# Kernel optimization log

Measured on AMD Instinct MI355X. Metric: run time of the kernel, lower is better.

Reference implementation:

```python
import jax, jax.numpy as jnp
import numpy as np

S, T, D, H = 16384, 16, 128, 3   # statements, AST nodes per statement, feat dim, heads
N = S * T
EPS = 1e-5


def setup_inputs() -> dict:
    key = jax.random.key(0)
    k = jax.random.split(key, 12)
    idx = np.arange(N)
    child = idx[idx % T != 0]                      # chain edges child->parent within each AST
    src = jnp.asarray(np.concatenate([child, idx]), dtype=jnp.int32)       # + self loops
    dst = jnp.asarray(np.concatenate([child - 1, idx]), dtype=jnp.int32)
    sD = 1.0 / np.sqrt(D)
    s3D = 1.0 / np.sqrt(3.0 * D)
    return dict(
        x=jax.random.normal(k[0], (N, D), jnp.float32),
        W0=jax.random.normal(k[1], (D, H * D), jnp.float32) * sD,
        a_src0=jax.random.normal(k[2], (H, D), jnp.float32) * sD,
        a_dst0=jax.random.normal(k[3], (H, D), jnp.float32) * sD,
        b0=jnp.zeros((H * D,), jnp.float32),
        g0=jnp.ones((H * D,), jnp.float32),
        be0=jnp.zeros((H * D,), jnp.float32),
        W1=jax.random.normal(k[4], (H * D, D), jnp.float32) * s3D,
        a_src1=jax.random.normal(k[5], (1, D), jnp.float32) * sD,
        a_dst1=jax.random.normal(k[6], (1, D), jnp.float32) * sD,
        b1=jnp.zeros((D,), jnp.float32),
        g1=jnp.ones((D,), jnp.float32),
        be1=jnp.zeros((D,), jnp.float32),
        p=jax.random.normal(k[7], (D,), jnp.float32),
        mW1=jax.random.normal(k[8], (D, 32), jnp.float32) * sD,
        mb1=jnp.zeros((32,), jnp.float32),
        mW2=jax.random.normal(k[9], (32, D), jnp.float32) / np.sqrt(32.0),
        mb2=jnp.zeros((D,), jnp.float32),
        src=src,
        dst=dst,
    )


def _gat(x, W, a_s, a_d, b, src, dst, heads, out_c):
    # PyG GATConv (concat heads, leaky_relu 0.2, self-loops already in edge list)
    h = (x @ W).reshape(-1, heads, out_c)                 # [N,H,C]
    al_s = jnp.einsum('nhc,hc->nh', h, a_s)
    al_d = jnp.einsum('nhc,hc->nh', h, a_d)
    e = jax.nn.leaky_relu(al_s[src] + al_d[dst], 0.2)     # [E,H]
    m = jax.ops.segment_max(e, dst, num_segments=N)       # segment softmax over incoming edges
    ex = jnp.exp(e - m[dst])
    den = jax.ops.segment_sum(ex, dst, num_segments=N)
    alpha = ex / den[dst]
    out = jax.ops.segment_sum(alpha[:, :, None] * h[src], dst, num_segments=N)
    return out.reshape(-1, heads * out_c) + b


def _bn(x, g, b):
    mu = x.mean(0)
    var = x.var(0)
    return (x - mu) * jax.lax.rsqrt(var + EPS) * g + b


def reference(x, W0, a_src0, a_dst0, b0, g0, be0, W1, a_src1, a_dst1, b1, g1, be1, p, mW1, mb1, mW2, mb2, src, dst):
    h = _bn(jax.nn.relu(_gat(x, W0, a_src0, a_dst0, b0, src, dst, H, D)), g0, be0)
    h = _bn(jax.nn.relu(_gat(h, W1, a_src1, a_dst1, b1, src, dst, 1, D)), g1, be1)
    # TopKPooling (default ratio=0.5) per statement AST of T nodes
    s = (h @ p) / (jnp.linalg.norm(p) + 1e-16)            # [N]
    s = s.reshape(S, T)
    k = T // 2
    vals, idxk = jax.lax.top_k(s, k)                      # [S,k]
    hr = h.reshape(S, T, D)
    sel = jnp.take_along_axis(hr, idxk[:, :, None], axis=1) * jnp.tanh(vals)[:, :, None]
    pooled = jax.nn.relu(sel).mean(axis=1)                # [S,D] readout of kept nodes
    out = jax.nn.relu(pooled @ mW1 + mb1) @ mW2 + mb2     # MLP 128->32->128
    return out
```

## Files before the change

kernel.cpp:

```cpp
#include <hip/hip_runtime.h>
#include <math.h>

#define N_NODES 262144
#define SSTMT   16384
#define TT      16
#define DD      128
#define HH      3
#define HD      384
#define EPSV    1e-5f

__device__ __forceinline__ void stage64x128(float (*dst)[128], const float* __restrict__ src)
{
    const int tid = threadIdx.x;
    #pragma unroll
    for (int j = 0; j < 8; ++j) {
        int gi = j * 256 + tid;
        int row = gi >> 5;
        int col = (gi & 31) * 4;
        *reinterpret_cast<float4*>(&dst[row][col]) =
            *reinterpret_cast<const float4*>(&src[(size_t)row * DD + col]);
    }
}

#define FMA16(av, b0, b1, b2, b3, ai)                                   \
    acc[ai][0] += av.x * b0.x; acc[ai][1] += av.x * b0.y;               \
    acc[ai][2] += av.x * b0.z; acc[ai][3] += av.x * b0.w;               \
    acc[ai][0] += av.y * b1.x; acc[ai][1] += av.y * b1.y;               \
    acc[ai][2] += av.y * b1.z; acc[ai][3] += av.y * b1.w;               \
    acc[ai][0] += av.z * b2.x; acc[ai][1] += av.z * b2.y;               \
    acc[ai][2] += av.z * b2.z; acc[ai][3] += av.z * b2.w;               \
    acc[ai][0] += av.w * b3.x; acc[ai][1] += av.w * b3.y;               \
    acc[ai][2] += av.w * b3.z; acc[ai][3] += av.w * b3.w;

template<int BSTR>
__device__ __forceinline__ void gemm128_lA(const float (*A)[128],
                                           const float* __restrict__ Bg,
                                           int rg, int c4, float acc[8][4])
{
    const float* bp = Bg + c4;
    #pragma unroll 4
    for (int k = 0; k < 128; k += 4) {
        float4 b0 = *reinterpret_cast<const float4*>(bp);
        float4 b1 = *reinterpret_cast<const float4*>(bp + BSTR);
        float4 b2 = *reinterpret_cast<const float4*>(bp + 2 * BSTR);
        float4 b3 = *reinterpret_cast<const float4*>(bp + 3 * BSTR);
        bp += 4 * BSTR;
        #pragma unroll
        for (int i = 0; i < 8; ++i) {
            float4 av = *reinterpret_cast<const float4*>(&A[rg * 8 + i][k]);
            FMA16(av, b0, b1, b2, b3, i)
        }
    }
}

__device__ __forceinline__ void attn_reg(const float acc[8][4],
                                         float4 av_s, float4 av_d,
                                         int rg, float aS[8], float aN[8])
{
    float als_t[8], ald_t[8];
    #pragma unroll
    for (int i = 0; i < 8; ++i) {
        als_t[i] = acc[i][0] * av_s.x + acc[i][1] * av_s.y
                 + acc[i][2] * av_s.z + acc[i][3] * av_s.w;
        ald_t[i] = acc[i][0] * av_d.x + acc[i][1] * av_d.y
                 + acc[i][2] * av_d.z + acc[i][3] * av_d.w;
    }
    #pragma unroll
    for (int m = 1; m <= 16; m <<= 1) {
        #pragma unroll
        for (int i = 0; i < 8; ++i) {
            als_t[i] += __shfl_xor(als_t[i], m);
            ald_t[i] += __shfl_xor(ald_t[i], m);
        }
    }
    float alsN = __shfl_down(als_t[0], 32);
    const bool rgodd = (rg & 1);
    #pragma unroll
    for (int i = 0; i < 8; ++i) {
        float es = als_t[i] + ald_t[i];
        es = es > 0.f ? es : 0.2f * es;
        float aSv = 1.f, aNv = 0.f;
        if (!(rgodd && i == 7)) {
            float en = ((i < 7) ? als_t[i + 1] : alsN) + ald_t[i];
            en = en > 0.f ? en : 0.2f * en;
            float mx = fmaxf(es, en);
            float xse = expf(es - mx), xne = expf(en - mx);
            float den = xse + xne;
            aSv = xse / den; aNv = xne / den;
        }
        aS[i] = aSv; aN[i] = aNv;
    }
}

__global__ __launch_bounds__(256, 4)
void gat0_stats(const float* __restrict__ x, const float* __restrict__ W0,
                const float* __restrict__ as0, const float* __restrict__ ad0,
                const float* __restrict__ b0, float* __restrict__ pA0)
{
    __shared__ float xs[64][128];

    const int tid = threadIdx.x;
    const int bid = blockIdx.x;
    const int rg = tid >> 5;
    const int c4 = (tid & 31) * 4;
    const size_t rb = (size_t)bid * 64;

    stage64x128(xs, x + rb * DD);
    __syncthreads();

    float psum[HH][4], qsum[HH][4];
    #pragma unroll
    for (int h = 0; h < HH; ++h)
        #pragma unroll
        for (int j = 0; j < 4; ++j) { psum[h][j] = 0.f; qsum[h][j] = 0.f; }

    for (int h = 0; h < HH; ++h) {
        float acc[8][4];
        #pragma unroll
        for (int i = 0; i < 8; ++i)
            #pragma unroll
            for (int j = 0; j < 4; ++j) acc[i][j] = 0.f;

        gemm128_lA<HD>(xs, W0 + h * DD, rg, c4, acc);

        float4 avS = *reinterpret_cast<const float4*>(&as0[h * DD + c4]);
        float4 avD = *reinterpret_cast<const float4*>(&ad0[h * DD + c4]);
        float aS[8], aN[8];
        attn_reg(acc, avS, avD, rg, aS, aN);

        float accN[4];
        #pragma unroll
        for (int j = 0; j < 4; ++j) accN[j] = __shfl_down(acc[0][j], 32);

        float4 bb = *reinterpret_cast<const float4*>(&b0[h * DD + c4]);
        float bbv[4] = {bb.x, bb.y, bb.z, bb.w};
        const bool rgodd = (rg & 1);
        #pragma unroll
        for (int i = 0; i < 8; ++i) {
            #pragma unroll
            for (int j = 0; j < 4; ++j) {
                float nbj = (i < 7) ? acc[i + 1][j] : (rgodd ? 0.f : accN[j]);
                float o = fmaxf(aS[i] * acc[i][j] + aN[i] * nbj + bbv[j], 0.f);
                psum[h][j] += o; qsum[h][j] += o * o;
            }
        }
    }

    float* bna = &xs[0][0];
    for (int h = 0; h < HH; ++h) {
        __syncthreads();
        #pragma unroll
        for (int j = 0; j < 4; ++j) {
            float s = psum[h][j] + __shfl_down(psum[h][j], 32);
            float q = qsum[h][j] + __shfl_down(qsum[h][j], 32);
            if ((tid & 63) < 32) {
                int w = tid >> 6;
                bna[w * 128 + c4 + j] = s;
                bna[512 + w * 128 + c4 + j] = q;
            }
        }
        __syncthreads();
        if (tid < 128) {
            float s = bna[tid] + bna[128 + tid] + bna[256 + tid] + bna[384 + tid];
            float q = bna[512 + tid] + bna[640 + tid] + bna[768 + tid] + bna[896 + tid];
            size_t idx = ((size_t)bid * HD + h * DD + tid) * 2;
            pA0[idx] = s; pA0[idx + 1] = q;
        }
    }
}

__global__ __launch_bounds__(256, 2)
void gat1_recomp(const float* __restrict__ x, const float* __restrict__ W0,
                 const float* __restrict__ as0, const float* __restrict__ ad0,
                 const float* __restrict__ b0, const float* __restrict__ sc0,
                 const float* __restrict__ sh0, const float* __restrict__ W1,
                 const float* __restrict__ as1, const float* __restrict__ ad1,
                 const float* __restrict__ b1,
                 float* __restrict__ r1, float* __restrict__ pA1)
{
    __shared__ float xs[64][128];
    __shared__ float hs[64][128];

    const int tid = threadIdx.x;
    const int bid = blockIdx.x;
    const int rg = tid >> 5;
    const int c4 = (tid & 31) * 4;
    const size_t rb = (size_t)bid * 64;
    const bool rgodd = (rg & 1);

    stage64x128(xs, x + rb * DD);
    __syncthreads();

    float acc2[8][4];
    #pragma unroll
    for (int i = 0; i < 8; ++i)
        #pragma unroll
        for (int j = 0; j < 4; ++j) acc2[i][j] = 0.f;

    for (int h = 0; h < HH; ++h) {
        float acc[8][4];
        #pragma unroll
        for (int i = 0; i < 8; ++i)
            #pragma unroll
            for (int j = 0; j < 4; ++j) acc[i][j] = 0.f;

        gemm128_lA<HD>(xs, W0 + h * DD, rg, c4, acc);

        float4 avS = *reinterpret_cast<const float4*>(&as0[h * DD + c4]);
        float4 avD = *reinterpret_cast<const float4*>(&ad0[h * DD + c4]);
        float aS[8], aN[8];
        attn_reg(acc, avS, avD, rg, aS, aN);

        float accN[4];
        #pragma unroll
        for (int j = 0; j < 4; ++j) accN[j] = __shfl_down(acc[0][j], 32);

        float4 bb  = *reinterpret_cast<const float4*>(&b0[h * DD + c4]);
        float4 scv = *reinterpret_cast<const float4*>(&sc0[h * DD + c4]);
        float4 shv = *reinterpret_cast<const float4*>(&sh0[h * DD + c4]);
        float bbv[4]  = {bb.x, bb.y, bb.z, bb.w};
        float scvv[4] = {scv.x, scv.y, scv.z, scv.w};
        float shvv[4] = {shv.x, shv.y, shv.z, shv.w};
        float rr[8][4];
        #pragma unroll
        for (int i = 0; i < 8; ++i) {
            #pragma unroll
            for (int j = 0; j < 4; ++j) {
                float nbj = (i < 7) ? acc[i + 1][j] : (rgodd ? 0.f : accN[j]);
                float o = fmaxf(aS[i] * acc[i][j] + aN[i] * nbj + bbv[j], 0.f);
                rr[i][j] = o * scvv[j] + shvv[j];
            }
        }

        __syncthreads();
        #pragma unroll
        for (int i = 0; i < 8; ++i) {
            float4 v; v.x = rr[i][0]; v.y = rr[i][1]; v.z = rr[i][2]; v.w = rr[i][3];
            *reinterpret_cast<float4*>(&hs[rg * 8 + i][c4]) = v;
        }
        __syncthreads();

        gemm128_lA<DD>(hs, W1 + (size_t)h * DD * DD, rg, c4, acc2);
    }

    float4 avS1 = *reinterpret_cast<const float4*>(&as1[c4]);
    float4 avD1 = *reinterpret_cast<const float4*>(&ad1[c4]);
    float aS[8], aN[8];
    attn_reg(acc2, avS1, avD1, rg, aS, aN);

    float accN[4];
    #pragma unroll
    for (int j = 0; j < 4; ++j) accN[j] = __shfl_down(acc2[0][j], 32);

    float4 bb1 = *reinterpret_cast<const float4*>(&b1[c4]);
    float bb1v[4] = {bb1.x, bb1.y, bb1.z, bb1.w};
    float ps1[4] = {0, 0, 0, 0}, pq1[4] = {0, 0, 0, 0};
    #pragma unroll
    for (int i = 0; i < 8; ++i) {
        float ov[4];
        #pragma unroll
        for (int j = 0; j < 4; ++j) {
            float nbj = (i < 7) ? acc2[i + 1][j] : (rgodd ? 0.f : accN[j]);
            float o = fmaxf(aS[i] * acc2[i][j] + aN[i] * nbj + bb1v[j], 0.f);
            ov[j] = o;
            ps1[j] += o; pq1[j] += o * o;
        }
        float4 v; v.x = ov[0]; v.y = ov[1]; v.z = ov[2]; v.w = ov[3];
        *reinterpret_cast<float4*>(&r1[(rb + rg * 8 + i) * DD + c4]) = v;
    }

    float* bna = &xs[0][0];
    __syncthreads();
    #pragma unroll
    for (int j = 0; j < 4; ++j) {
        float s = ps1[j] + __shfl_down(ps1[j], 32);
        float q = pq1[j] + __shfl_down(pq1[j], 32);
        if ((tid & 63) < 32) {
            int w = tid >> 6;
            bna[w * 128 + c4 + j] = s;
            bna[512 + w * 128 + c4 + j] = q;
        }
    }
    __syncthreads();
    if (tid < 128) {
        float s = bna[tid] + bna[128 + tid] + bna[256 + tid] + bna[384 + tid];
        float q = bna[512 + tid] + bna[640 + tid] + bna[768 + tid] + bna[896 + tid];
        size_t idx = ((size_t)bid * DD + tid) * 2;
        pA1[idx] = s; pA1[idx + 1] = q;
    }
}

__global__ __launch_bounds__(256)
void bn_reduce(const float* __restrict__ pA, int nblk, int ncol, float invN,
               const float* __restrict__ g, const float* __restrict__ be,
               float* __restrict__ sc, float* __restrict__ sh)
{
    __shared__ float rs[256], rq[256];
    int col = blockIdx.x, tid = threadIdx.x;
    float s = 0.f, q = 0.f;
    for (int i = tid; i < nblk; i += 256) {
        size_t idx = ((size_t)i * ncol + col) * 2;
        s += pA[idx]; q += pA[idx + 1];
    }
    rs[tid] = s; rq[tid] = q;
    __syncthreads();
    for (int o = 128; o > 0; o >>= 1) {
        if (tid < o) { rs[tid] += rs[tid + o]; rq[tid] += rq[tid + o]; }
        __syncthreads();
    }
    if (tid == 0) {
        float mu  = rs[0] * invN;
        float var = fmaxf(rq[0] * invN - mu * mu, 0.f);
        float inv = 1.0f / sqrtf(var + EPSV);
        float scv = g[col] * inv;
        sc[col] = scv;
        sh[col] = be[col] - mu * scv;
    }
}

__global__ __launch_bounds__(128)
void compute_pn(const float* __restrict__ p, float* __restrict__ pn)
{
    __shared__ float rs[128];
    int t = threadIdx.x;
    float v = p[t];
    rs[t] = v * v;
    __syncthreads();
    for (int o = 64; o > 0; o >>= 1) {
        if (t < o) rs[t] += rs[t + o];
        __syncthreads();
    }
    float nrm = sqrtf(rs[0]) + 1e-16f;
    pn[t] = v / nrm;
}

__global__ __launch_bounds__(128)
void pool_mlp(const float* __restrict__ r1, const float* __restrict__ sc1,
              const float* __restrict__ sh1, const float* __restrict__ pn,
              const float* __restrict__ mW1, const float* __restrict__ mb1,
              const float* __restrict__ mW2, const float* __restrict__ mb2,
              float* __restrict__ out)
{
    __shared__ float hf[16][136];
    __shared__ float sv[16];
    __shared__ float tv[16];
    __shared__ float pooled[128];
    __shared__ float y1[32];
    int tid = threadIdx.x;
    int sid = blockIdx.x;
    float scv = sc1[tid], shv = sh1[tid];
    const float* base = r1 + (size_t)sid * TT * DD;
    #pragma unroll
    for (int i = 0; i < 16; ++i)
        hf[i][tid] = base[i * DD + tid] * scv + shv;
    __syncthreads();

    {
        int r = tid >> 3, q = tid & 7;
        float s = 0.f;
        #pragma unroll
        for (int cc = 0; cc < 16; ++cc) {
            int c = q + cc * 8;
            s += hf[r][c] * pn[c];
        }
        s += __shfl_down(s, 4, 8);
        s += __shfl_down(s, 2, 8);
        s += __shfl_down(s, 1, 8);
        if (q == 0) sv[r] = s;
    }
    __syncthreads();

    if (tid < 16) {
        float si = sv[tid];
        int rank = 0;
        #pragma unroll
        for (int u = 0; u < 16; ++u) {
            float su = sv[u];
            rank += (su > si || (su == si && u < tid)) ? 1 : 0;
        }
        tv[tid] = (rank < 8) ? tanhf(si) : 0.f;
    }
    __syncthreads();

    {
        float a = 0.f;
        #pragma unroll
        for (int rr = 0; rr < 16; ++rr)
            a += fmaxf(hf[rr][tid] * tv[rr], 0.f);
        pooled[tid] = a * 0.125f;
    }
    __syncthreads();

    {
        int j = tid >> 2, q = tid & 3;
        float a = 0.f;
        #pragma unroll
        for (int cc = 0; cc < 32; ++cc) {
            int c = q + cc * 4;
            a += pooled[c] * mW1[(size_t)c * 32 + j];
        }
        a += __shfl_down(a, 2, 4);
        a += __shfl_down(a, 1, 4);
        if (q == 0) y1[j] = fmaxf(a + mb1[j], 0.f);
    }
    __syncthreads();

    {
        float o = mb2[tid];
        #pragma unroll
        for (int j = 0; j < 32; ++j) o += y1[j] * mW2[j * 128 + tid];
        out[(size_t)sid * 128 + tid] = o;
    }
}

extern "C" void kernel_launch(void* const* d_in, const int* in_sizes, int n_in,
                              void* d_out, int out_size, void* d_ws, size_t ws_size,
                              hipStream_t stream)
{
    (void)in_sizes; (void)n_in; (void)out_size; (void)ws_size;
    const float* x   = (const float*)d_in[0];
    const float* W0  = (const float*)d_in[1];
    const float* as0 = (const float*)d_in[2];
    const float* ad0 = (const float*)d_in[3];
    const float* b0  = (const float*)d_in[4];
    const float* g0  = (const float*)d_in[5];
    const float* be0 = (const float*)d_in[6];
    const float* W1  = (const float*)d_in[7];
    const float* as1 = (const float*)d_in[8];
    const float* ad1 = (const float*)d_in[9];
    const float* b1  = (const float*)d_in[10];
    const float* g1  = (const float*)d_in[11];
    const float* be1 = (const float*)d_in[12];
    const float* p   = (const float*)d_in[13];
    const float* mW1 = (const float*)d_in[14];
    const float* mb1 = (const float*)d_in[15];
    const float* mW2 = (const float*)d_in[16];
    const float* mb2 = (const float*)d_in[17];
    float* out = (float*)d_out;

    const size_t R1B  = (size_t)N_NODES * DD * 4;
    const size_t PA0B = 4096ull * HD * 2 * 4;
    const size_t PA1B = 4096ull * DD * 2 * 4;

    char* ws = (char*)d_ws;
    float* r1  = (float*)ws;
    float* pA0 = (float*)(ws + R1B);
    float* pA1 = (float*)(ws + R1B + PA0B);
    float* vec = (float*)(ws + R1B + PA0B + PA1B);
    float* sc0 = vec;
    float* sh0 = vec + 512;
    float* sc1 = vec + 1024;
    float* sh1 = vec + 1536;
    float* pn  = vec + 2048;

    const float invN = 1.0f / (float)N_NODES;

    gat0_stats<<<N_NODES / 64, 256, 0, stream>>>(x, W0, as0, ad0, b0, pA0);
    bn_reduce<<<HD, 256, 0, stream>>>(pA0, N_NODES / 64, HD, invN, g0, be0, sc0, sh0);
    compute_pn<<<1, 128, 0, stream>>>(p, pn);
    gat1_recomp<<<N_NODES / 64, 256, 0, stream>>>(x, W0, as0, ad0, b0, sc0, sh0,
                                                  W1, as1, ad1, b1, r1, pA1);
    bn_reduce<<<DD, 256, 0, stream>>>(pA1, N_NODES / 64, DD, invN, g1, be1, sc1, sh1);
    pool_mlp<<<SSTMT, 128, 0, stream>>>(r1, sc1, sh1, pn, mW1, mb1, mW2, mb2, out);
}
```

Baseline: 1.296 ms.

## Use 8x8 register tiles with swizzled LDS and split-K in GAT kernels

Reworks the two fused GAT kernels so each thread computes an 8x8 output tile instead of 8x4, giving more FMAs per shared-memory and global load. The staged x and h tiles now use an XOR swizzle to avoid LDS bank conflicts. gat0_stats runs with 128 threads, and gat1_recomp splits K across two thread halves whose partial sums are combined through shared memory. This raises register pressure, adds extra barriers and split-K reduction traffic, and leaves only half the threads doing the attention epilogue in the second kernel.

```diff
diff --git a/kernel.cpp b/kernel.cpp
--- a/kernel.cpp
+++ b/kernel.cpp
@@ -9,163 +9,174 @@
 #define HD      384
 #define EPSV    1e-5f
 
-__device__ __forceinline__ void stage64x128(float (*dst)[128], const float* __restrict__ src)
+__device__ __forceinline__ int swzc(int row, int c) { return c ^ (((row >> 3) & 3) << 2); }
+
+template<int NTHR>
+__device__ __forceinline__ void stageSwz(float (*dst)[DD], const float* __restrict__ src)
 {
     const int tid = threadIdx.x;
     #pragma unroll
-    for (int j = 0; j < 8; ++j) {
-        int gi = j * 256 + tid;
+    for (int j = 0; j < 2048 / NTHR; ++j) {
+        int gi = j * NTHR + tid;
         int row = gi >> 5;
-        int col = (gi & 31) * 4;
-        *reinterpret_cast<float4*>(&dst[row][col]) =
-            *reinterpret_cast<const float4*>(&src[(size_t)row * DD + col]);
-    }
-}
-
-#define FMA16(av, b0, b1, b2, b3, ai)                                   \
-    acc[ai][0] += av.x * b0.x; acc[ai][1] += av.x * b0.y;               \
-    acc[ai][2] += av.x * b0.z; acc[ai][3] += av.x * b0.w;               \
-    acc[ai][0] += av.y * b1.x; acc[ai][1] += av.y * b1.y;               \
-    acc[ai][2] += av.y * b1.z; acc[ai][3] += av.y * b1.w;               \
-    acc[ai][0] += av.z * b2.x; acc[ai][1] += av.z * b2.y;               \
-    acc[ai][2] += av.z * b2.z; acc[ai][3] += av.z * b2.w;               \
-    acc[ai][0] += av.w * b3.x; acc[ai][1] += av.w * b3.y;               \
-    acc[ai][2] += av.w * b3.z; acc[ai][3] += av.w * b3.w;
-
-template<int BSTR>
-__device__ __forceinline__ void gemm128_lA(const float (*A)[128],
-                                           const float* __restrict__ Bg,
-                                           int rg, int c4, float acc[8][4])
-{
-    const float* bp = Bg + c4;
-    #pragma unroll 4
-    for (int k = 0; k < 128; k += 4) {
-        float4 b0 = *reinterpret_cast<const float4*>(bp);
-        float4 b1 = *reinterpret_cast<const float4*>(bp + BSTR);
-        float4 b2 = *reinterpret_cast<const float4*>(bp + 2 * BSTR);
-        float4 b3 = *reinterpret_cast<const float4*>(bp + 3 * BSTR);
-        bp += 4 * BSTR;
+        int c4 = (gi & 31) * 4;
+        *reinterpret_cast<float4*>(&dst[row][swzc(row, c4)]) =
+            *reinterpret_cast<const float4*>(&src[(size_t)row * DD + c4]);
+    }
+}
+
+template<int BSTR, int KLEN>
+__device__ __forceinline__ void gemm8x8(const float (*A)[DD], const float* __restrict__ Bbase,
+                                        int kbeg, int rr, int pad, float acc[8][8])
+{
+    const float* bp = Bbase + (size_t)kbeg * BSTR;
+    const float* ar = &A[rr * 8][0];
+    #pragma unroll 2
+    for (int k = 0; k < KLEN; k += 4) {
+        float4 b00 = *reinterpret_cast<const float4*>(bp);
+        float4 b01 = *reinterpret_cast<const float4*>(bp + 4);
+        float4 b10 = *reinterpret_cast<const float4*>(bp + BSTR);
+        float4 b11 = *reinterpret_cast<const float4*>(bp + BSTR + 4);
+        float4 b20 = *reinterpret_cast<const float4*>(bp + 2 * BSTR);
+        float4 b21 = *reinterpret_cast<const float4*>(bp + 2 * BSTR + 4);
+        float4 b30 = *reinterpret_cast<const float4*>(bp + 3 * BSTR);
+        float4 b31 = *reinterpret_cast<const float4*>(bp + 3 * BSTR + 4);
+        bp += 4 * (size_t)BSTR;
+        const int pc = (kbeg + k) ^ pad;
         #pragma unroll
         for (int i = 0; i < 8; ++i) {
-            float4 av = *reinterpret_cast<const float4*>(&A[rg * 8 + i][k]);
-            FMA16(av, b0, b1, b2, b3, i)
-        }
-    }
-}
-
-__device__ __forceinline__ void attn_reg(const float acc[8][4],
-                                         float4 av_s, float4 av_d,
-                                         int rg, float aS[8], float aN[8])
-{
-    float als_t[8], ald_t[8];
+            float4 a = *reinterpret_cast<const float4*>(ar + i * DD + pc);
+            acc[i][0] += a.x*b00.x; acc[i][1] += a.x*b00.y; acc[i][2] += a.x*b00.z; acc[i][3] += a.x*b00.w;
+            acc[i][4] += a.x*b01.x; acc[i][5] += a.x*b01.y; acc[i][6] += a.x*b01.z; acc[i][7] += a.x*b01.w;
+            acc[i][0] += a.y*b10.x; acc[i][1] += a.y*b10.y; acc[i][2] += a.y*b10.z; acc[i][3] += a.y*b10.w;
+            acc[i][4] += a.y*b11.x; acc[i][5] += a.y*b11.y; acc[i][6] += a.y*b11.z; acc[i][7] += a.y*b11.w;
+            acc[i][0] += a.z*b20.x; acc[i][1] += a.z*b20.y; acc[i][2] += a.z*b20.z; acc[i][3] += a.z*b20.w;
+            acc[i][4] += a.z*b21.x; acc[i][5] += a.z*b21.y; acc[i][6] += a.z*b21.z; acc[i][7] += a.z*b21.w;
+            acc[i][0] += a.w*b30.x; acc[i][1] += a.w*b30.y; acc[i][2] += a.w*b30.z; acc[i][3] += a.w*b30.w;
+            acc[i][4] += a.w*b31.x; acc[i][5] += a.w*b31.y; acc[i][6] += a.w*b31.z; acc[i][7] += a.w*b31.w;
+        }
+    }
+}
+
+__device__ __forceinline__ void attnAgg(float acc[8][8],
+                                        const float* __restrict__ avsP,
+                                        const float* __restrict__ avdP,
+                                        const float* __restrict__ bP, int rr)
+{
+    float4 s0 = *reinterpret_cast<const float4*>(avsP);
+    float4 s1 = *reinterpret_cast<const float4*>(avsP + 4);
+    float4 d0 = *reinterpret_cast<const float4*>(avdP);
+    float4 d1 = *reinterpret_cast<const float4*>(avdP + 4);
+    float als[8], ald[8];
     #pragma unroll
     for (int i = 0; i < 8; ++i) {
-        als_t[i] = acc[i][0] * av_s.x + acc[i][1] * av_s.y
-                 + acc[i][2] * av_s.z + acc[i][3] * av_s.w;
-        ald_t[i] = acc[i][0] * av_d.x + acc[i][1] * av_d.y
-                 + acc[i][2] * av_d.z + acc[i][3] * av_d.w;
-    }
-    #pragma unroll
-    for (int m = 1; m <= 16; m <<= 1) {
+        als[i] = acc[i][0]*s0.x + acc[i][1]*s0.y + acc[i][2]*s0.z + acc[i][3]*s0.w
+               + acc[i][4]*s1.x + acc[i][5]*s1.y + acc[i][6]*s1.z + acc[i][7]*s1.w;
+        ald[i] = acc[i][0]*d0.x + acc[i][1]*d0.y + acc[i][2]*d0.z + acc[i][3]*d0.w
+               + acc[i][4]*d1.x + acc[i][5]*d1.y + acc[i][6]*d1.z + acc[i][7]*d1.w;
+    }
+    #pragma unroll
+    for (int m = 1; m <= 8; m <<= 1) {
         #pragma unroll
         for (int i = 0; i < 8; ++i) {
-            als_t[i] += __shfl_xor(als_t[i], m);
-            ald_t[i] += __shfl_xor(ald_t[i], m);
-        }
-    }
-    float alsN = __shfl_down(als_t[0], 32);
-    const bool rgodd = (rg & 1);
+            als[i] += __shfl_xor(als[i], m);
+            ald[i] += __shfl_xor(ald[i], m);
+        }
+    }
+    float alsN = __shfl_down(als[0], 16);
+    float accN[8];
+    #pragma unroll
+    for (int j = 0; j < 8; ++j) accN[j] = __shfl_down(acc[0][j], 16);
+
+    float4 bb0 = *reinterpret_cast<const float4*>(bP);
+    float4 bb1 = *reinterpret_cast<const float4*>(bP + 4);
+    float bbv[8] = {bb0.x, bb0.y, bb0.z, bb0.w, bb1.x, bb1.y, bb1.z, bb1.w};
+    const bool tail7 = (rr & 1);
     #pragma unroll
     for (int i = 0; i < 8; ++i) {
-        float es = als_t[i] + ald_t[i];
+        float es = als[i] + ald[i];
         es = es > 0.f ? es : 0.2f * es;
-        float aSv = 1.f, aNv = 0.f;
-        if (!(rgodd && i == 7)) {
-            float en = ((i < 7) ? als_t[i + 1] : alsN) + ald_t[i];
+        float aS = 1.f, aN = 0.f;
+        if (!(tail7 && i == 7)) {
+            float en = ((i < 7) ? als[i + 1] : alsN) + ald[i];
             en = en > 0.f ? en : 0.2f * en;
             float mx = fmaxf(es, en);
-            float xse = expf(es - mx), xne = expf(en - mx);
-            float den = xse + xne;
-            aSv = xse / den; aNv = xne / den;
-        }
-        aS[i] = aSv; aN[i] = aNv;
-    }
-}
-
-__global__ __launch_bounds__(256, 4)
+            float e1 = expf(es - mx), e2 = expf(en - mx);
+            float den = e1 + e2;
+            aS = e1 / den; aN = e2 / den;
+        }
+        #pragma unroll
+        for (int j = 0; j < 8; ++j) {
+            float nb = (i < 7) ? acc[i + 1][j] : accN[j];
+            acc[i][j] = fmaxf(aS * acc[i][j] + aN * nb + bbv[j], 0.f);
+        }
+    }
+}
+
+__global__ __launch_bounds__(128, 2)
 void gat0_stats(const float* __restrict__ x, const float* __restrict__ W0,
                 const float* __restrict__ as0, const float* __restrict__ ad0,
                 const float* __restrict__ b0, float* __restrict__ pA0)
 {
-    __shared__ float xs[64][128];
+    __shared__ float xs[64][DD];
+    __shared__ float bns[8][DD];
 
     const int tid = threadIdx.x;
     const int bid = blockIdx.x;
-    const int rg = tid >> 5;
-    const int c4 = (tid & 31) * 4;
+    const int rr = tid >> 4;
+    const int cg = tid & 15;
+    const int pad = (rr & 3) << 2;
     const size_t rb = (size_t)bid * 64;
 
-    stage64x128(xs, x + rb * DD);
-    __syncthreads();
-
-    float psum[HH][4], qsum[HH][4];
+    stageSwz<128>(xs, x + rb * DD);
+    __syncthreads();
+
+    float psum[HH][8], qsum[HH][8];
     #pragma unroll
     for (int h = 0; h < HH; ++h)
         #pragma unroll
-        for (int j = 0; j < 4; ++j) { psum[h][j] = 0.f; qsum[h][j] = 0.f; }
+        for (int j = 0; j < 8; ++j) { psum[h][j] = 0.f; qsum[h][j] = 0.f; }
 
     for (int h = 0; h < HH; ++h) {
-        float acc[8][4];
+        float acc[8][8];
         #pragma unroll
         for (int i = 0; i < 8; ++i)
             #pragma unroll
-            for (int j = 0; j < 4; ++j) acc[i][j] = 0.f;
-
-        gemm128_lA<HD>(xs, W0 + h * DD, rg, c4, acc);
-
-        float4 avS = *reinterpret_cast<const float4*>(&as0[h * DD + c4]);
-        float4 avD = *reinterpret_cast<const float4*>(&ad0[h * DD + c4]);
-        float aS[8], aN[8];
-        attn_reg(acc, avS, avD, rg, aS, aN);
-
-        float accN[4];
-        #pragma unroll
-        for (int j = 0; j < 4; ++j) accN[j] = __shfl_down(acc[0][j], 32);
-
-        float4 bb = *reinterpret_cast<const float4*>(&b0[h * DD + c4]);
-        float bbv[4] = {bb.x, bb.y, bb.z, bb.w};
-        const bool rgodd = (rg & 1);
-        #pragma unroll
-        for (int i = 0; i < 8; ++i) {
-            #pragma unroll
-            for (int j = 0; j < 4; ++j) {
-                float nbj = (i < 7) ? acc[i + 1][j] : (rgodd ? 0.f : accN[j]);
-                float o = fmaxf(aS[i] * acc[i][j] + aN[i] * nbj + bbv[j], 0.f);
+            for (int j = 0; j < 8; ++j) acc[i][j] = 0.f;
+
+        gemm8x8<HD, 128>(xs, W0 + h * DD + cg * 8, 0, rr, pad, acc);
+        attnAgg(acc, as0 + h * DD + cg * 8, ad0 + h * DD + cg * 8, b0 + h * DD + cg * 8, rr);
+
+        #pragma unroll
+        for (int i = 0; i < 8; ++i)
+            #pragma unroll
+            for (int j = 0; j < 8; ++j) {
+                float o = acc[i][j];
                 psum[h][j] += o; qsum[h][j] += o * o;
             }
-        }
-    }
-
-    float* bna = &xs[0][0];
+    }
+
     for (int h = 0; h < HH; ++h) {
         __syncthreads();
-        #pragma unroll
-        for (int j = 0; j < 4; ++j) {
-            float s = psum[h][j] + __shfl_down(psum[h][j], 32);
-            float q = qsum[h][j] + __shfl_down(qsum[h][j], 32);
-            if ((tid & 63) < 32) {
-                int w = tid >> 6;
-                bna[w * 128 + c4 + j] = s;
-                bna[512 + w * 128 + c4 + j] = q;
-            }
-        }
-        __syncthreads();
-        if (tid < 128) {
-            float s = bna[tid] + bna[128 + tid] + bna[256 + tid] + bna[384 + tid];
-            float q = bna[512 + tid] + bna[640 + tid] + bna[768 + tid] + bna[896 + tid];
-            size_t idx = ((size_t)bid * HD + h * DD + tid) * 2;
-            pA0[idx] = s; pA0[idx + 1] = q;
-        }
+        *reinterpret_cast<float4*>(&bns[rr][cg * 8]) =
+            make_float4(psum[h][0], psum[h][1], psum[h][2], psum[h][3]);
+        *reinterpret_cast<float4*>(&bns[rr][cg * 8 + 4]) =
+            make_float4(psum[h][4], psum[h][5], psum[h][6], psum[h][7]);
+        __syncthreads();
+        float sv = 0.f;
+        #pragma unroll
+        for (int w = 0; w < 8; ++w) sv += bns[w][tid];
+        __syncthreads();
+        *reinterpret_cast<float4*>(&bns[rr][cg * 8]) =
+            make_float4(qsum[h][0], qsum[h][1], qsum[h][2], qsum[h][3]);
+        *reinterpret_cast<float4*>(&bns[rr][cg * 8 + 4]) =
+            make_float4(qsum[h][4], qsum[h][5], qsum[h][6], qsum[h][7]);
+        __syncthreads();
+        float qv = 0.f;
+        #pragma unroll
+        for (int w = 0; w < 8; ++w) qv += bns[w][tid];
+        size_t idx = ((size_t)bid * HD + h * DD + tid) * 2;
+        pA0[idx] = sv; pA0[idx + 1] = qv;
     }
 }
 
@@ -178,113 +189,129 @@
                  const float* __restrict__ b1,
                  float* __restrict__ r1, float* __restrict__ pA1)
 {
-    __shared__ float xs[64][128];
-    __shared__ float hs[64][128];
+    __shared__ float xs[64][DD];
+    __shared__ float hs[64][DD];
+    __shared__ float bps[8][DD], bqs[8][DD];
 
     const int tid = threadIdx.x;
     const int bid = blockIdx.x;
-    const int rg = tid >> 5;
-    const int c4 = (tid & 31) * 4;
+    const int kh = tid >> 7;
+    const int rr = (tid >> 4) & 7;
+    const int cg = tid & 15;
+    const int pad = (rr & 3) << 2;
     const size_t rb = (size_t)bid * 64;
-    const bool rgodd = (rg & 1);
-
-    stage64x128(xs, x + rb * DD);
-    __syncthreads();
-
-    float acc2[8][4];
+
+    stageSwz<256>(xs, x + rb * DD);
+    __syncthreads();
+
+    float acc2[8][8];
     #pragma unroll
     for (int i = 0; i < 8; ++i)
         #pragma unroll
-        for (int j = 0; j < 4; ++j) acc2[i][j] = 0.f;
+        for (int j = 0; j < 8; ++j) acc2[i][j] = 0.f;
 
     for (int h = 0; h < HH; ++h) {
-        float acc[8][4];
+        float acc[8][8];
         #pragma unroll
         for (int i = 0; i < 8; ++i)
             #pragma unroll
-            for (int j = 0; j < 4; ++j) acc[i][j] = 0.f;
-
-        gemm128_lA<HD>(xs, W0 + h * DD, rg, c4, acc);
-
-        float4 avS = *reinterpret_cast<const float4*>(&as0[h * DD + c4]);
-        float4 avD = *reinterpret_cast<const float4*>(&ad0[h * DD + c4]);
-        float aS[8], aN[8];
-        attn_reg(acc, avS, avD, rg, aS, aN);
-
-        float accN[4];
-        #pragma unroll
-        for (int j = 0; j < 4; ++j) accN[j] = __shfl_down(acc[0][j], 32);
-
-        float4 bb  = *reinterpret_cast<const float4*>(&b0[h * DD + c4]);
-        float4 scv = *reinterpret_cast<const float4*>(&sc0[h * DD + c4]);
-        float4 shv = *reinterpret_cast<const float4*>(&sh0[h * DD + c4]);
-        float bbv[4]  = {bb.x, bb.y, bb.z, bb.w};
-        float scvv[4] = {scv.x, scv.y, scv.z, scv.w};
-        float shvv[4] = {shv.x, shv.y, shv.z, shv.w};
-        float rr[8][4];
+            for (int j = 0; j < 8; ++j) acc[i][j] = 0.f;
+
+        gemm8x8<HD, 64>(xs, W0 + h * DD + cg * 8, kh * 64, rr, pad, acc);
+
+        __syncthreads();
+        if (kh == 1) {
+            #pragma unroll
+            for (int i = 0; i < 8; ++i) {
+                int pc = (cg * 8) ^ pad;
+                *reinterpret_cast<float4*>(&hs[rr * 8 + i][pc]) =
+                    make_float4(acc[i][0], acc[i][1], acc[i][2], acc[i][3]);
+                *reinterpret_cast<float4*>(&hs[rr * 8 + i][pc ^ 4]) =
+                    make_float4(acc[i][4], acc[i][5], acc[i][6], acc[i][7]);
+            }
+        }
+        __syncthreads();
+        if (kh == 0) {
+            #pragma unroll
+            for (int i = 0; i < 8; ++i) {
+                int pc = (cg * 8) ^ pad;
+                float4 p0 = *reinterpret_cast<const float4*>(&hs[rr * 8 + i][pc]);
+                float4 p1 = *reinterpret_cast<const float4*>(&hs[rr * 8 + i][pc ^ 4]);
+                acc[i][0] += p0.x; acc[i][1] += p0.y; acc[i][2] += p0.z; acc[i][3] += p0.w;
+                acc[i][4] += p1.x; acc[i][5] += p1.y; acc[i][6] += p1.z; acc[i][7] += p1.w;
+            }
+            attnAgg(acc, as0 + h * DD + cg * 8, ad0 + h * DD + cg * 8, b0 + h * DD + cg * 8, rr);
+            float4 sc0a = *reinterpret_cast<const float4*>(&sc0[h * DD + cg * 8]);
+            float4 sc0b = *reinterpret_cast<const float4*>(&sc0[h * DD + cg * 8 + 4]);
+            float4 sh0a = *reinterpret_cast<const float4*>(&sh0[h * DD + cg * 8]);
+            float4 sh0b = *reinterpret_cast<const float4*>(&sh0[h * DD + cg * 8 + 4]);
+            float scv[8] = {sc0a.x, sc0a.y, sc0a.z, sc0a.w, sc0b.x, sc0b.y, sc0b.z, sc0b.w};
+            float shv[8] = {sh0a.x, sh0a.y, sh0a.z, sh0a.w, sh0b.x, sh0b.y, sh0b.z, sh0b.w};
+            #pragma unroll
+            for (int i = 0; i < 8; ++i) {
+                int pc = (cg * 8) ^ pad;
+                float v0 = acc[i][0] * scv[0] + shv[0];
+                float v1 = acc[i][1] * scv[1] + shv[1];
+                float v2 = acc[i][2] * scv[2] + shv[2];
+                float v3 = acc[i][3] * scv[3] + shv[3];
+                float v4 = acc[i][4] * scv[4] + shv[4];
+                float v5 = acc[i][5] * scv[5] + shv[5];
+                float v6 = acc[i][6] * scv[6] + shv[6];
+                float v7 = acc[i][7] * scv[7] + shv[7];
+                *reinterpret_cast<float4*>(&hs[rr * 8 + i][pc]) = make_float4(v0, v1, v2, v3);
+                *reinterpret_cast<float4*>(&hs[rr * 8 + i][pc ^ 4]) = make_float4(v4, v5, v6, v7);
+            }
+        }
+        __syncthreads();
+
+        gemm8x8<DD, 64>(hs, W1 + (size_t)(h * DD) * DD + cg * 8, kh * 64, rr, pad, acc2);
+    }
+
+    __syncthreads();
+    if (kh == 1) {
         #pragma unroll
         for (int i = 0; i < 8; ++i) {
-            #pragma unroll
-            for (int j = 0; j < 4; ++j) {
-                float nbj = (i < 7) ? acc[i + 1][j] : (rgodd ? 0.f : accN[j]);
-                float o = fmaxf(aS[i] * acc[i][j] + aN[i] * nbj + bbv[j], 0.f);
-                rr[i][j] = o * scvv[j] + shvv[j];
-            }
-        }
-
-        __syncthreads();
+            int pc = (cg * 8) ^ pad;
+            *reinterpret_cast<float4*>(&xs[rr * 8 + i][pc]) =
+                make_float4(acc2[i][0], acc2[i][1], acc2[i][2], acc2[i][3]);
+            *reinterpret_cast<float4*>(&xs[rr * 8 + i][pc ^ 4]) =
+                make_float4(acc2[i][4], acc2[i][5], acc2[i][6], acc2[i][7]);
+        }
+    }
+    __syncthreads();
+    if (kh == 0) {
         #pragma unroll
         for (int i = 0; i < 8; ++i) {
-            float4 v; v.x = rr[i][0]; v.y = rr[i][1]; v.z = rr[i][2]; v.w = rr[i][3];
-            *reinterpret_cast<float4*>(&hs[rg * 8 + i][c4]) = v;
-        }
-        __syncthreads();
-
-        gemm128_lA<DD>(hs, W1 + (size_t)h * DD * DD, rg, c4, acc2);
-    }
-
-    float4 avS1 = *reinterpret_cast<const float4*>(&as1[c4]);
-    float4 avD1 = *reinterpret_cast<const float4*>(&ad1[c4]);
-    float aS[8], aN[8];
-    attn_reg(acc2, avS1, avD1, rg, aS, aN);
-
-    float accN[4];
-    #pragma unroll
-    for (int j = 0; j < 4; ++j) accN[j] = __shfl_down(acc2[0][j], 32);
-
-    float4 bb1 = *reinterpret_cast<const float4*>(&b1[c4]);
-    float bb1v[4] = {bb1.x, bb1.y, bb1.z, bb1.w};
-    float ps1[4] = {0, 0, 0, 0}, pq1[4] = {0, 0, 0, 0};
-    #pragma unroll
-    for (int i = 0; i < 8; ++i) {
-        float ov[4];
-        #pragma unroll
-        for (int j = 0; j < 4; ++j) {
-            float nbj = (i < 7) ? acc2[i + 1][j] : (rgodd ? 0.f : accN[j]);
-            float o = fmaxf(aS[i] * acc2[i][j] + aN[i] * nbj + bb1v[j], 0.f);
-            ov[j] = o;
-            ps1[j] += o; pq1[j] += o * o;
-        }
-        float4 v; v.x = ov[0]; v.y = ov[1]; v.z = ov[2]; v.w = ov[3];
-        *reinterpret_cast<float4*>(&r1[(rb + rg * 8 + i) * DD + c4]) = v;
-    }
-
-    float* bna = &xs[0][0];
-    __syncthreads();
-    #pragma unroll
-    for (int j = 0; j < 4; ++j) {
-        float s = ps1[j] + __shfl_down(ps1[j], 32);
-        float q = pq1[j] + __shfl_down(pq1[j], 32);
-        if ((tid & 63) < 32) {
-            int w = tid >> 6;
-            bna[w * 128 + c4 + j] = s;
-            bna[512 + w * 128 + c4 + j] = q;
-        }
+            int pc = (cg * 8) ^ pad;
+            float4 p0 = *reinterpret_cast<const float4*>(&xs[rr * 8 + i][pc]);
+            float4 p1 = *reinterpret_cast<const float4*>(&xs[rr * 8 + i][pc ^ 4]);
+            acc2[i][0] += p0.x; acc2[i][1] += p0.y; acc2[i][2] += p0.z; acc2[i][3] += p0.w;
+            acc2[i][4] += p1.x; acc2[i][5] += p1.y; acc2[i][6] += p1.z; acc2[i][7] += p1.w;
+        }
+        attnAgg(acc2, as1 + cg * 8, ad1 + cg * 8, b1 + cg * 8, rr);
+
+        float ps[8], pq[8];
+        #pragma unroll
+        for (int j = 0; j < 8; ++j) { ps[j] = 0.f; pq[j] = 0.f; }
+        #pragma unroll
+        for (int i = 0; i < 8; ++i) {
+            *reinterpret_cast<float4*>(&r1[(rb + rr * 8 + i) * DD + cg * 8]) =
+                make_float4(acc2[i][0], acc2[i][1], acc2[i][2], acc2[i][3]);
+            *reinterpret_cast<float4*>(&r1[(rb + rr * 8 + i) * DD + cg * 8 + 4]) =
+                make_float4(acc2[i][4], acc2[i][5], acc2[i][6], acc2[i][7]);
+            #pragma unroll
+            for (int j = 0; j < 8; ++j) { ps[j] += acc2[i][j]; pq[j] += acc2[i][j] * acc2[i][j]; }
+        }
+        *reinterpret_cast<float4*>(&bps[rr][cg * 8])     = make_float4(ps[0], ps[1], ps[2], ps[3]);
+        *reinterpret_cast<float4*>(&bps[rr][cg * 8 + 4]) = make_float4(ps[4], ps[5], ps[6], ps[7]);
+        *reinterpret_cast<float4*>(&bqs[rr][cg * 8])     = make_float4(pq[0], pq[1], pq[2], pq[3]);
+        *reinterpret_cast<float4*>(&bqs[rr][cg * 8 + 4]) = make_float4(pq[4], pq[5], pq[6], pq[7]);
     }
     __syncthreads();
     if (tid < 128) {
-        float s = bna[tid] + bna[128 + tid] + bna[256 + tid] + bna[384 + tid];
-        float q = bna[512 + tid] + bna[640 + tid] + bna[768 + tid] + bna[896 + tid];
+        float s = 0.f, q = 0.f;
+        #pragma unroll
+        for (int w = 0; w < 8; ++w) { s += bps[w][tid]; q += bqs[w][tid]; }
         size_t idx = ((size_t)bid * DD + tid) * 2;
         pA1[idx] = s; pA1[idx + 1] = q;
     }
@@ -385,8 +412,8 @@
     {
         float a = 0.f;
         #pragma unroll
-        for (int rr = 0; rr < 16; ++rr)
-            a += fmaxf(hf[rr][tid] * tv[rr], 0.f);
+        for (int rr2 = 0; rr2 < 16; ++rr2)
+            a += fmaxf(hf[rr2][tid] * tv[rr2], 0.f);
         pooled[tid] = a * 0.125f;
     }
     __syncthreads();
@@ -455,7 +482,7 @@
 
     const float invN = 1.0f / (float)N_NODES;
 
-    gat0_stats<<<N_NODES / 64, 256, 0, stream>>>(x, W0, as0, ad0, b0, pA0);
+    gat0_stats<<<N_NODES / 64, 128, 0, stream>>>(x, W0, as0, ad0, b0, pA0);
     bn_reduce<<<HD, 256, 0, stream>>>(pA0, N_NODES / 64, HD, invN, g0, be0, sc0, sh0);
     compute_pn<<<1, 128, 0, stream>>>(p, pn);
     gat1_recomp<<<N_NODES / 64, 256, 0, stream>>>(x, W0, as0, ad0, b0, sc0, sh0,
```

Measured after the change: 1.117 ms. 13.8% less time.
